# Optimization experiments

Measured on AMD Instinct MI355X. Metric: run time of the kernel, lower is better.

## Reference

```python
import jax, jax.numpy as jnp
import numpy as np

NR = 116  # number of AAL ROIs
VOL = (61, 73, 61)
V = 61 * 73 * 61


def setup_inputs() -> dict:
    B, C, D, T = 8, 192, 2, 24  # batch MUST be 8: fc1 outputs 64 = B*B
    key = jax.random.key(0)
    ks = jax.random.split(key, 16)
    s = 0.02
    # synthetic AAL template: every voxel gets a ROI label 0..115, all present
    rng = np.random.default_rng(0)
    labels_np = rng.integers(0, NR, size=V).astype(np.int32)
    labels_np[:NR] = np.arange(NR)
    # ROI centroid pairwise distances (compute_node_distances equivalent)
    coords = np.stack(np.meshgrid(np.arange(61), np.arange(73), np.arange(61), indexing='ij'), -1).reshape(V, 3).astype(np.float64)
    cent = np.zeros((NR, 3))
    for r in range(NR):
        cent[r] = coords[labels_np == r].mean(0)
    dist = np.linalg.norm(cent[:, None] - cent[None, :], axis=-1).astype(np.float32)
    return {
        'x': jax.random.normal(ks[0], (B, C, D, D, D, T), jnp.float32),
        'roi_labels': jnp.asarray(labels_np.reshape(VOL)),
        'node_distances': jnp.asarray(dist),
        'fc_w': s * jax.random.normal(ks[1], (V, C * D * D * D), jnp.float32),
        'fc_b': jnp.zeros((V,), jnp.float32),
        'fs_w1': s * jax.random.normal(ks[2], (NR, 64), jnp.float32),
        'fs_b1': jnp.zeros((NR, 64), jnp.float32),
        'fs_w2': s * jax.random.normal(ks[3], (NR, 64, 64), jnp.float32),
        'fs_b2': jnp.zeros((NR, 64), jnp.float32),
        'fs_w3': s * jax.random.normal(ks[4], (NR, 64), jnp.float32),
        'fs_b3': jnp.zeros((NR,), jnp.float32),
        'm_w1': s * jax.random.normal(ks[5], (64,), jnp.float32),
        'm_b1': jnp.zeros((64,), jnp.float32),
        'm_w2': s * jax.random.normal(ks[6], (64, 64), jnp.float32),
        'm_b2': jnp.zeros((64,), jnp.float32),
        'm_w3': s * jax.random.normal(ks[7], (64,), jnp.float32),
        'm_b3': jnp.zeros((1,), jnp.float32),
        'fc1_w': s * jax.random.normal(ks[8], (64, NR * NR), jnp.float32),
        'fc1_b': jnp.zeros((64,), jnp.float32),
        'hidden_w': s * jax.random.normal(ks[9], (768, 192 + NR), jnp.float32),
        'hidden_b': jnp.zeros((768,), jnp.float32),
        'out_w': s * jax.random.normal(ks[10], (1, 768), jnp.float32),
        'out_b': jnp.zeros((1,), jnp.float32),
    }


def _forward(x, node_distances, fc_w, fc_b, fs_w1, fs_b1, fs_w2, fs_b2, fs_w3, fs_b3,
             m_w1, m_b1, m_w2, m_b2, m_w3, m_b3, fc1_w, fc1_b,
             hidden_w, hidden_b, out_w, out_b, labels):
    B, T = x.shape[0], x.shape[-1]
    # fc projects each time frame into the 61x73x61 volume: [B,T,V]
    xt = jnp.swapaxes(x.reshape(B, -1, T), 1, 2)            # [B,T,1536]
    vox = jnp.einsum('bti,vi->btv', xt, fc_w) + fc_b        # [B,T,V]
    # ROI time series = segment-mean of voxels per ROI (replaces python loops)
    seg = jax.ops.segment_sum(jnp.moveaxis(vox, 2, 0).reshape(V, B * T), labels, num_segments=NR)
    cnt = jax.ops.segment_sum(jnp.ones((V,), vox.dtype), labels, num_segments=NR)
    ts = (seg / jnp.maximum(cnt, 1.0)[:, None]).reshape(NR, B, T)
    x_node = ts.mean(axis=2).T                              # [B,116]
    # 116 tiny per-ROI MLPs, vectorized (eval mode: dropout is identity)
    h = jax.nn.relu(x_node[..., None] * fs_w1[None] + fs_b1[None])       # [B,116,64]
    h = jax.nn.relu(jnp.einsum('bni,noi->bno', h, fs_w2) + fs_b2[None])  # [B,116,64]
    fx = jnp.einsum('bni,ni->bn', h, fs_w3) + fs_b3[None]                # [B,116]
    # distance MLP m over all 116*116 pairwise distances
    d = node_distances.reshape(-1, 1)                       # [13456,1]
    g = jax.nn.relu(d * m_w1[None, :] + m_b1)
    g = jax.nn.relu(g @ m_w2.T + m_b2)
    md = (g @ m_w3[:, None] + m_b3).reshape(-1)             # [13456]
    mmat = (fc1_w @ md + fc1_b).reshape(B, B)               # requires B*B == 64
    mf = mmat @ fx                                          # [B,116]
    # avgpool branch: mean over all spatial*time positions -> [B,192]
    pooled = x.reshape(B, x.shape[1], -1).mean(axis=2)
    cat = jnp.concatenate([mf, pooled], axis=1)             # [B,308]
    hid = cat @ hidden_w.T + hidden_b                       # no activation (as in source)
    return hid @ out_w.T + out_b                            # [B,1]


def reference(x, roi_labels, node_distances, fc_w, fc_b, fs_w1, fs_b1, fs_w2, fs_b2, fs_w3, fs_b3,
              m_w1, m_b1, m_w2, m_b2, m_w3, m_b3, fc1_w, fc1_b, hidden_w, hidden_b, out_w, out_b):
    return _forward(x, node_distances, fc_w, fc_b, fs_w1, fs_b1, fs_w2, fs_b2, fs_w3, fs_b3,
                    m_w1, m_b1, m_w2, m_b2, m_w3, m_b3, fc1_w, fc1_b,
                    hidden_w, hidden_b, out_w, out_b, roi_labels.reshape(-1))
```

## Files before the change

kernel.cpp:

```cpp
#include <hip/hip_runtime.h>

#define V_TOT 271633
#define NRR 116
#define CIN 1536
#define T_LEN 24
#define B_SZ 8
#define NP (NRR*NRR)
#define CATN 308
#define SPLITS 44
#define NST (NRR*SPLITS)
#define VB 1062
#define WPAD 310
#define DPS 12
#define DISTB 2243
#define MEGA_STREAM_BASE (DISTB + 8)

typedef float nfloat4 __attribute__((ext_vector_type(4)));

__global__ __launch_bounds__(256) void hist_xbar_kernel(const int* __restrict__ labels,
                                                        int* __restrict__ blockHist,
                                                        const float* __restrict__ x,
                                                        float* __restrict__ xbar) {
    if (blockIdx.x < VB) {
        __shared__ int h[NRR];
        for (int i = threadIdx.x; i < NRR; i += 256) h[i] = 0;
        __syncthreads();
        int v = blockIdx.x * 256 + threadIdx.x;
        if (v < V_TOT) atomicAdd(&h[labels[v]], 1);
        __syncthreads();
        for (int i = threadIdx.x; i < NRR; i += 256)
            blockHist[(size_t)i * VB + blockIdx.x] = h[i];
    } else {
        int idx = (blockIdx.x - VB) * 256 + threadIdx.x;
        if (idx < B_SZ * CIN) {
            const float* p = x + (size_t)idx * T_LEN;
            float s = 0.f;
            #pragma unroll
            for (int t = 0; t < T_LEN; ++t) s += p[t];
            xbar[idx] = s * (1.0f / T_LEN);
        }
    }
}

__global__ __launch_bounds__(256) void binscan_kernel(const int* __restrict__ blockHist,
                                                      int* __restrict__ blockBase,
                                                      int* __restrict__ counts) {
    const int r = blockIdx.x;
    const int lane = threadIdx.x & 63, w = threadIdx.x >> 6;
    __shared__ int wsum[4];
    int run = 0;
    for (int base = 0; base < VB; base += 256) {
        const int i = base + threadIdx.x;
        const int orig = (i < VB) ? blockHist[(size_t)r * VB + i] : 0;
        int val = orig;
        #pragma unroll
        for (int off = 1; off < 64; off <<= 1) {
            int t = __shfl_up(val, off);
            if (lane >= off) val += t;
        }
        if (lane == 63) wsum[w] = val;
        __syncthreads();
        int woff = 0;
        #pragma unroll
        for (int j = 0; j < 4; ++j) if (j < w) woff += wsum[j];
        if (i < VB) blockBase[(size_t)r * VB + i] = run + woff + val - orig;
        int tot = wsum[0] + wsum[1] + wsum[2] + wsum[3];
        __syncthreads();
        run += tot;
    }
    if (threadIdx.x == 0) counts[r] = run;
}

__global__ void offsets_kernel(const int* __restrict__ counts, int* __restrict__ offsets) {
    if (threadIdx.x == 0) {
        int acc = 0;
        for (int r = 0; r < NRR; ++r) { offsets[r] = acc; acc += counts[r]; }
        offsets[NRR] = acc;
    }
}

__global__ __launch_bounds__(256) void scatter_kernel(const int* __restrict__ labels,
                                                      const int* __restrict__ offsets,
                                                      const int* __restrict__ blockBase,
                                                      int* __restrict__ perm) {
    __shared__ int lab[256];
    const int v = blockIdx.x * 256 + threadIdx.x;
    const int r = (v < V_TOT) ? labels[v] : -1;
    lab[threadIdx.x] = r;
    __syncthreads();
    if (r >= 0) {
        int rank = 0;
        for (int t = 0; t < (int)threadIdx.x; ++t) rank += (lab[t] == r);
        perm[offsets[r] + blockBase[(size_t)r * VB + blockIdx.x] + rank] = v;
    }
}

__device__ __forceinline__ void add4(float4& a, const float4 b) {
    a.x += b.x; a.y += b.y; a.z += b.z; a.w += b.w;
}
__device__ __forceinline__ float4 ldnt4(const float* p) {
    nfloat4 v = __builtin_nontemporal_load((const nfloat4*)p);
    return make_float4(v.x, v.y, v.z, v.w);
}

__global__ __launch_bounds__(384, 6) void mega_kernel(
        const float* __restrict__ fc_w, const float* __restrict__ fc_b,
        const int* __restrict__ perm,
        const int* __restrict__ counts, const int* __restrict__ offsets,
        const float* __restrict__ xbar, float* __restrict__ dotpart,
        const float* __restrict__ dist,
        const float* __restrict__ mw1, const float* __restrict__ mb1,
        const float* __restrict__ mw2, const float* __restrict__ mb2,
        const float* __restrict__ mw3, const float* __restrict__ mb3,
        float* __restrict__ md,
        const float* __restrict__ hidden_w, const float* __restrict__ hidden_b,
        const float* __restrict__ out_w, const float* __restrict__ out_b,
        float* __restrict__ weffpart) {
    const int bid = blockIdx.x;
    const int lane = threadIdx.x & 63, w = threadIdx.x >> 6;

    if (bid < DISTB) {
        const int p = bid * 6 + w;
        if (p < NP) {
            float d = dist[p];
            float g1 = fmaxf(d * mw1[lane] + mb1[lane], 0.f);
            const float* w2row = mw2 + lane * 64;
            float acc = mb2[lane];
            #pragma unroll
            for (int i = 0; i < 64; ++i) acc += __shfl(g1, i) * w2row[i];
            float g2 = fmaxf(acc, 0.f);
            float t = g2 * mw3[lane];
            for (int s = 32; s > 0; s >>= 1) t += __shfl_down(t, s);
            if (lane == 0) md[p] = t + mb3[0];
        }
        return;
    }
    if (bid < MEGA_STREAM_BASE) {
        const int jb = bid - DISTB;
        const int k = threadIdx.x;
        const int j0 = jb * 96, j1 = j0 + 96;
        if (k < CATN) {
            float s = 0.f;
            for (int j = j0; j < j1; ++j) s += hidden_w[(size_t)j * CATN + k] * out_w[j];
            weffpart[jb*WPAD + k] = s;
        } else if (k == CATN) {
            float s = 0.f;
            for (int j = j0; j < j1; ++j) s += hidden_b[j] * out_w[j];
            weffpart[jb*WPAD + CATN] = s + (jb == 0 ? out_b[0] : 0.f);
        }
        return;
    }

    const int sbid = bid - MEGA_STREAM_BASE;
    const int r = sbid / SPLITS, s = sbid % SPLITS;
    const int n = counts[r], off = offsets[r];
    const int chunk = (n + SPLITS - 1) / SPLITS;
    const int k0 = min(s * chunk, n);
    const int k1 = min(k0 + chunk, n);
    const int c4 = threadIdx.x * 4;

    float4 a0{0,0,0,0}, a1{0,0,0,0}, a2{0,0,0,0}, a3{0,0,0,0};
    float4 a4{0,0,0,0}, a5{0,0,0,0}, a6{0,0,0,0}, a7{0,0,0,0};
    int k = k0;
    for (; k + 8 <= k1; k += 8) {
        const int v0 = perm[off+k+0], v1 = perm[off+k+1], v2 = perm[off+k+2], v3 = perm[off+k+3];
        const int v4 = perm[off+k+4], v5 = perm[off+k+5], v6 = perm[off+k+6], v7 = perm[off+k+7];
        const float4 x0 = ldnt4(fc_w + (size_t)v0*CIN + c4);
        const float4 x1 = ldnt4(fc_w + (size_t)v1*CIN + c4);
        const float4 x2 = ldnt4(fc_w + (size_t)v2*CIN + c4);
        const float4 x3 = ldnt4(fc_w + (size_t)v3*CIN + c4);
        const float4 x4 = ldnt4(fc_w + (size_t)v4*CIN + c4);
        const float4 x5 = ldnt4(fc_w + (size_t)v5*CIN + c4);
        const float4 x6 = ldnt4(fc_w + (size_t)v6*CIN + c4);
        const float4 x7 = ldnt4(fc_w + (size_t)v7*CIN + c4);
        add4(a0, x0); add4(a1, x1); add4(a2, x2); add4(a3, x3);
        add4(a4, x4); add4(a5, x5); add4(a6, x6); add4(a7, x7);
    }
    for (; k < k1; ++k) {
        const int v = perm[off+k];
        add4(a0, ldnt4(fc_w + (size_t)v*CIN + c4));
    }
    add4(a0, a1); add4(a2, a3); add4(a4, a5); add4(a6, a7);
    add4(a0, a2); add4(a4, a6); add4(a0, a4);

    float bacc = 0.f;
    for (int kk = k0 + threadIdx.x; kk < k1; kk += 384) bacc += fc_b[perm[off+kk]];

    float d[B_SZ];
    #pragma unroll
    for (int b = 0; b < B_SZ; ++b) {
        const float4 xb = *(const float4*)(xbar + b*CIN + c4);
        d[b] = a0.x*xb.x + a0.y*xb.y + a0.z*xb.z + a0.w*xb.w;
    }
    __shared__ float red[6][9];
    #pragma unroll
    for (int b = 0; b < B_SZ; ++b) {
        float v = d[b];
        for (int sft = 32; sft > 0; sft >>= 1) v += __shfl_down(v, sft);
        if (lane == 0) red[w][b] = v;
    }
    {
        float v = bacc;
        for (int sft = 32; sft > 0; sft >>= 1) v += __shfl_down(v, sft);
        if (lane == 0) red[w][8] = v;
    }
    __syncthreads();
    if (threadIdx.x < 9) {
        float v = 0.f;
        #pragma unroll
        for (int j = 0; j < 6; ++j) v += red[j][threadIdx.x];
        dotpart[((size_t)(r*SPLITS + s))*DPS + threadIdx.x] = v;
    }
}

__global__ __launch_bounds__(256) void mid_kernel(
        const float* __restrict__ dotpart, const int* __restrict__ counts,
        const float* __restrict__ w1, const float* __restrict__ b1,
        const float* __restrict__ w2, const float* __restrict__ b2,
        const float* __restrict__ w3, const float* __restrict__ b3,
        float* __restrict__ fx,
        const float* __restrict__ fc1_w, const float* __restrict__ md,
        float* __restrict__ mmatpart) {
    const int bid = blockIdx.x;
    const int lane = threadIdx.x & 63;
    if (bid < 232) {
        int w = bid * 4 + (threadIdx.x >> 6);
        int b = w / NRR, r = w % NRR;
        float sdot = 0.f, sb = 0.f;
        if (lane < SPLITS) {
            const float* p = dotpart + ((size_t)(r*SPLITS + lane))*DPS;
            sdot = p[b]; sb = p[8];
        }
        #pragma unroll
        for (int off = 32; off > 0; off >>= 1) {
            sdot += __shfl_xor(sdot, off);
            sb   += __shfl_xor(sb, off);
        }
        float xn = (sdot + sb) / (float)counts[r];

        float h1 = fmaxf(xn * w1[r*64 + lane] + b1[r*64 + lane], 0.f);
        const float* w2row = w2 + ((size_t)r*64 + lane) * 64;
        float acc = b2[r*64 + lane];
        #pragma unroll
        for (int i = 0; i < 64; ++i) acc += __shfl(h1, i) * w2row[i];
        float h2 = fmaxf(acc, 0.f);
        float p = h2 * w3[r*64 + lane];
        for (int sft = 32; sft > 0; sft >>= 1) p += __shfl_down(p, sft);
        if (lane == 0) fx[b * NRR + r] = p + b3[r];
    } else {
        const int fb = bid - 232;
        const int j = fb >> 2, q = fb & 3;
        const int p0 = q * (NP/4), p1 = p0 + (NP/4);
        const float* row = fc1_w + (size_t)j * NP;
        float s = 0.f;
        for (int p = p0 + threadIdx.x; p < p1; p += 256) s += row[p] * md[p];
        __shared__ float red[4];
        for (int sft = 32; sft > 0; sft >>= 1) s += __shfl_down(s, sft);
        if ((threadIdx.x & 63) == 0) red[threadIdx.x >> 6] = s;
        __syncthreads();
        if (threadIdx.x == 0) mmatpart[j*4 + q] = red[0] + red[1] + red[2] + red[3];
    }
}

__global__ __launch_bounds__(512) void tail_kernel(const float* __restrict__ mmatpart,
                                                   const float* __restrict__ fc1_b,
                                                   const float* __restrict__ fx,
                                                   const float* __restrict__ xbar,
                                                   const float* __restrict__ weffpart,
                                                   float* __restrict__ out) {
    __shared__ float mmat[64];
    __shared__ float cat[B_SZ][CATN];
    if (threadIdx.x < 64) {
        const float* p = mmatpart + threadIdx.x*4;
        mmat[threadIdx.x] = p[0] + p[1] + p[2] + p[3] + fc1_b[threadIdx.x];
    }
    __syncthreads();
    for (int idx = threadIdx.x; idx < B_SZ * NRR; idx += 512) {
        int b = idx / NRR, r = idx % NRR;
        float s = 0.f;
        #pragma unroll
        for (int kk = 0; kk < 8; ++kk) s += mmat[b*8 + kk] * fx[kk * NRR + r];
        cat[b][r] = s;
    }
    for (int idx = threadIdx.x; idx < B_SZ * 192; idx += 512) {
        int b = idx / 192, c = idx % 192;
        float s = 0.f;
        #pragma unroll
        for (int j = 0; j < 8; ++j) s += xbar[b * CIN + c*8 + j];
        cat[b][NRR + c] = s * (1.0f / 8.0f);
    }
    __syncthreads();
    const int b = threadIdx.x >> 6, lane = threadIdx.x & 63;
    float s = 0.f;
    for (int k = lane; k < CATN; k += 64) {
        float wk = 0.f;
        #pragma unroll
        for (int jb = 0; jb < 8; ++jb) wk += weffpart[jb*WPAD + k];
        s += cat[b][k] * wk;
    }
    for (int sft = 32; sft > 0; sft >>= 1) s += __shfl_down(s, sft);
    if (lane == 0) {
        float beff = 0.f;
        #pragma unroll
        for (int jb = 0; jb < 8; ++jb) beff += weffpart[jb*WPAD + CATN];
        out[b] = s + beff;
    }
}

extern "C" void kernel_launch(void* const* d_in, const int* in_sizes, int n_in,
                              void* d_out, int out_size, void* d_ws, size_t ws_size,
                              hipStream_t stream) {
    const float* x        = (const float*)d_in[0];
    const int*   labels   = (const int*)d_in[1];
    const float* dist     = (const float*)d_in[2];
    const float* fc_w     = (const float*)d_in[3];
    const float* fc_b     = (const float*)d_in[4];
    const float* fs_w1    = (const float*)d_in[5];
    const float* fs_b1    = (const float*)d_in[6];
    const float* fs_w2    = (const float*)d_in[7];
    const float* fs_b2    = (const float*)d_in[8];
    const float* fs_w3    = (const float*)d_in[9];
    const float* fs_b3    = (const float*)d_in[10];
    const float* m_w1     = (const float*)d_in[11];
    const float* m_b1     = (const float*)d_in[12];
    const float* m_w2     = (const float*)d_in[13];
    const float* m_b2     = (const float*)d_in[14];
    const float* m_w3     = (const float*)d_in[15];
    const float* m_b3     = (const float*)d_in[16];
    const float* fc1_w    = (const float*)d_in[17];
    const float* fc1_b    = (const float*)d_in[18];
    const float* hidden_w = (const float*)d_in[19];
    const float* hidden_b = (const float*)d_in[20];
    const float* out_w    = (const float*)d_in[21];
    const float* out_b    = (const float*)d_in[22];
    float* out = (float*)d_out;

    int* counts    = (int*)d_ws;
    int* offsets   = counts + 128;
    int* blockHist = offsets + 128;
    int* blockBase = blockHist + NRR*VB;
    int* perm      = blockBase + NRR*VB;
    float* fb = (float*)(perm + ((V_TOT + 255) / 256) * 256);
    float* dotpart  = fb;  fb += (size_t)NRR * SPLITS * DPS;
    float* xbar     = fb;  fb += B_SZ * CIN;
    float* fx       = fb;  fb += B_SZ * NRR + 32;
    float* md       = fb;  fb += NP;
    float* mmatpart = fb;  fb += 256;
    float* weffpart = fb;  fb += 8 * WPAD;

    hist_xbar_kernel<<<VB + 48, 256, 0, stream>>>(labels, blockHist, x, xbar);
    binscan_kernel<<<NRR, 256, 0, stream>>>(blockHist, blockBase, counts);
    offsets_kernel<<<1, 64, 0, stream>>>(counts, offsets);
    scatter_kernel<<<VB, 256, 0, stream>>>(labels, offsets, blockBase, perm);
    mega_kernel<<<MEGA_STREAM_BASE + NST, 384, 0, stream>>>(
        fc_w, fc_b, perm, counts, offsets, xbar, dotpart,
        dist, m_w1, m_b1, m_w2, m_b2, m_w3, m_b3, md,
        hidden_w, hidden_b, out_w, out_b, weffpart);
    mid_kernel<<<488, 256, 0, stream>>>(dotpart, counts,
        fs_w1, fs_b1, fs_w2, fs_b2, fs_w3, fs_b3, fx, fc1_w, md, mmatpart);
    tail_kernel<<<1, 512, 0, stream>>>(mmatpart, fc1_b, fx, xbar, weffpart, out);
}
```

Baseline: 324.5 us.

## Interleave small MLP blocks with streaming blocks and fold offsets scan into consumers

Removes the single-thread offsets kernel by computing ROI prefix offsets with a wave-level shuffle scan inside scatter_kernel and mega_kernel. Reorders mega_kernel's grid into groups of 11 fc_w streaming blocks plus 5 small distance-MLP/weight-folding blocks so bandwidth-bound streaming starts immediately instead of after thousands of small blocks. Adds redundant per-wave scan work of counts in each streaming block.

```diff
diff --git a/kernel.cpp b/kernel.cpp
--- a/kernel.cpp
+++ b/kernel.cpp
@@ -13,7 +13,9 @@
 #define WPAD 310
 #define DPS 12
 #define DISTB 2243
-#define MEGA_STREAM_BASE (DISTB + 8)
+#define SMALLN (DISTB + 8)
+#define GROUPS 464
+#define MEGA_GRID (GROUPS * 16)
 
 typedef float nfloat4 __attribute__((ext_vector_type(4)));
 
@@ -71,27 +73,53 @@
     if (threadIdx.x == 0) counts[r] = run;
 }
 
-__global__ void offsets_kernel(const int* __restrict__ counts, int* __restrict__ offsets) {
-    if (threadIdx.x == 0) {
-        int acc = 0;
-        for (int r = 0; r < NRR; ++r) { offsets[r] = acc; acc += counts[r]; }
-        offsets[NRR] = acc;
-    }
+__device__ __forceinline__ void roi_off(const int* __restrict__ counts, int r,
+                                        int& off, int& n) {
+    const int lane = threadIdx.x & 63;
+    int a = counts[lane];
+    int b = (lane + 64 < NRR) ? counts[lane + 64] : 0;
+    int sa = a, sb = b;
+    #pragma unroll
+    for (int d = 1; d < 64; d <<= 1) {
+        int t = __shfl_up(sa, d); if (lane >= d) sa += t;
+        t = __shfl_up(sb, d);     if (lane >= d) sb += t;
+    }
+    const int tot_a = __shfl(sa, 63);
+    if (r == 0) off = 0;
+    else if (r < 64) off = __shfl(sa, r - 1);
+    else if (r == 64) off = tot_a;
+    else off = tot_a + __shfl(sb, r - 65);
+    n = counts[r];
 }
 
 __global__ __launch_bounds__(256) void scatter_kernel(const int* __restrict__ labels,
-                                                      const int* __restrict__ offsets,
+                                                      const int* __restrict__ counts,
                                                       const int* __restrict__ blockBase,
                                                       int* __restrict__ perm) {
     __shared__ int lab[256];
+    __shared__ int offs_s[NRR];
     const int v = blockIdx.x * 256 + threadIdx.x;
     const int r = (v < V_TOT) ? labels[v] : -1;
     lab[threadIdx.x] = r;
+    if (threadIdx.x < 64) {
+        const int lane = threadIdx.x;
+        int a = counts[lane];
+        int b = (lane + 64 < NRR) ? counts[lane + 64] : 0;
+        int sa = a, sb = b;
+        #pragma unroll
+        for (int d = 1; d < 64; d <<= 1) {
+            int t = __shfl_up(sa, d); if (lane >= d) sa += t;
+            t = __shfl_up(sb, d);     if (lane >= d) sb += t;
+        }
+        const int tot_a = __shfl(sa, 63);
+        offs_s[lane] = sa - a;
+        if (lane + 64 < NRR) offs_s[lane + 64] = tot_a + sb - b;
+    }
     __syncthreads();
     if (r >= 0) {
         int rank = 0;
         for (int t = 0; t < (int)threadIdx.x; ++t) rank += (lab[t] == r);
-        perm[offsets[r] + blockBase[(size_t)r * VB + blockIdx.x] + rank] = v;
+        perm[offs_s[r] + blockBase[(size_t)r * VB + blockIdx.x] + rank] = v;
     }
 }
 
@@ -105,8 +133,7 @@
 
 __global__ __launch_bounds__(384, 6) void mega_kernel(
         const float* __restrict__ fc_w, const float* __restrict__ fc_b,
-        const int* __restrict__ perm,
-        const int* __restrict__ counts, const int* __restrict__ offsets,
+        const int* __restrict__ perm, const int* __restrict__ counts,
         const float* __restrict__ xbar, float* __restrict__ dotpart,
         const float* __restrict__ dist,
         const float* __restrict__ mw1, const float* __restrict__ mb1,
@@ -116,44 +143,47 @@
         const float* __restrict__ hidden_w, const float* __restrict__ hidden_b,
         const float* __restrict__ out_w, const float* __restrict__ out_b,
         float* __restrict__ weffpart) {
-    const int bid = blockIdx.x;
+    const int g = blockIdx.x >> 4, m = blockIdx.x & 15;
     const int lane = threadIdx.x & 63, w = threadIdx.x >> 6;
 
-    if (bid < DISTB) {
-        const int p = bid * 6 + w;
-        if (p < NP) {
-            float d = dist[p];
-            float g1 = fmaxf(d * mw1[lane] + mb1[lane], 0.f);
-            const float* w2row = mw2 + lane * 64;
-            float acc = mb2[lane];
-            #pragma unroll
-            for (int i = 0; i < 64; ++i) acc += __shfl(g1, i) * w2row[i];
-            float g2 = fmaxf(acc, 0.f);
-            float t = g2 * mw3[lane];
-            for (int s = 32; s > 0; s >>= 1) t += __shfl_down(t, s);
-            if (lane == 0) md[p] = t + mb3[0];
+    if (m >= 11) {
+        const int idx = g * 5 + (m - 11);
+        if (idx >= SMALLN) return;
+        if (idx < DISTB) {
+            const int p = idx * 6 + w;
+            if (p < NP) {
+                float d = dist[p];
+                float g1 = fmaxf(d * mw1[lane] + mb1[lane], 0.f);
+                const float* w2row = mw2 + lane * 64;
+                float acc = mb2[lane];
+                #pragma unroll
+                for (int i = 0; i < 64; ++i) acc += __shfl(g1, i) * w2row[i];
+                float g2 = fmaxf(acc, 0.f);
+                float t = g2 * mw3[lane];
+                for (int s = 32; s > 0; s >>= 1) t += __shfl_down(t, s);
+                if (lane == 0) md[p] = t + mb3[0];
+            }
+        } else {
+            const int jb = idx - DISTB;
+            const int k = threadIdx.x;
+            const int j0 = jb * 96, j1 = j0 + 96;
+            if (k < CATN) {
+                float s = 0.f;
+                for (int j = j0; j < j1; ++j) s += hidden_w[(size_t)j * CATN + k] * out_w[j];
+                weffpart[jb*WPAD + k] = s;
+            } else if (k == CATN) {
+                float s = 0.f;
+                for (int j = j0; j < j1; ++j) s += hidden_b[j] * out_w[j];
+                weffpart[jb*WPAD + CATN] = s + (jb == 0 ? out_b[0] : 0.f);
+            }
         }
         return;
     }
-    if (bid < MEGA_STREAM_BASE) {
-        const int jb = bid - DISTB;
-        const int k = threadIdx.x;
-        const int j0 = jb * 96, j1 = j0 + 96;
-        if (k < CATN) {
-            float s = 0.f;
-            for (int j = j0; j < j1; ++j) s += hidden_w[(size_t)j * CATN + k] * out_w[j];
-            weffpart[jb*WPAD + k] = s;
-        } else if (k == CATN) {
-            float s = 0.f;
-            for (int j = j0; j < j1; ++j) s += hidden_b[j] * out_w[j];
-            weffpart[jb*WPAD + CATN] = s + (jb == 0 ? out_b[0] : 0.f);
-        }
-        return;
-    }
-
-    const int sbid = bid - MEGA_STREAM_BASE;
+
+    const int sbid = g * 11 + m;
     const int r = sbid / SPLITS, s = sbid % SPLITS;
-    const int n = counts[r], off = offsets[r];
+    int off, n;
+    roi_off(counts, r, off, n);
     const int chunk = (n + SPLITS - 1) / SPLITS;
     const int k0 = min(s * chunk, n);
     const int k1 = min(k0 + chunk, n);
@@ -336,8 +366,7 @@
     float* out = (float*)d_out;
 
     int* counts    = (int*)d_ws;
-    int* offsets   = counts + 128;
-    int* blockHist = offsets + 128;
+    int* blockHist = counts + 128;
     int* blockBase = blockHist + NRR*VB;
     int* perm      = blockBase + NRR*VB;
     float* fb = (float*)(perm + ((V_TOT + 255) / 256) * 256);
@@ -350,10 +379,9 @@
 
     hist_xbar_kernel<<<VB + 48, 256, 0, stream>>>(labels, blockHist, x, xbar);
     binscan_kernel<<<NRR, 256, 0, stream>>>(blockHist, blockBase, counts);
-    offsets_kernel<<<1, 64, 0, stream>>>(counts, offsets);
-    scatter_kernel<<<VB, 256, 0, stream>>>(labels, offsets, blockBase, perm);
-    mega_kernel<<<MEGA_STREAM_BASE + NST, 384, 0, stream>>>(
-        fc_w, fc_b, perm, counts, offsets, xbar, dotpart,
+    scatter_kernel<<<VB, 256, 0, stream>>>(labels, counts, blockBase, perm);
+    mega_kernel<<<MEGA_GRID, 384, 0, stream>>>(
+        fc_w, fc_b, perm, counts, xbar, dotpart,
         dist, m_w1, m_b1, m_w2, m_b2, m_w3, m_b3, md,
         hidden_w, hidden_b, out_w, out_b, weffpart);
     mid_kernel<<<488, 256, 0, stream>>>(dotpart, counts,
```

Result: slower. 368.4 us (+13.5%).
